# Kernel optimization log

Hardware: AMD Instinct MI355X
Metric: run time of the kernel (lower is better)

## Reference

```python
import jax, jax.numpy as jnp
import numpy as np

N = 20000   # nodes
E = 640000  # edges
F = 128     # input feature dim
H1 = 64     # hidden1
H2 = 32     # hidden2 (forced by Bilinear(32,32,1))
R = 65      # num_relations / num classes
B = 4096    # query pairs


def rgcn_conv(x, src, dst, etype, W, Wroot, b):
    """PyG RGCNConv with aggr='mean': out_i = sum_r mean_{j in N_r(i)} x_j @ W_r + x_i @ Wroot + b."""
    n, f = x.shape
    seg = dst * R + etype                      # combined (node, relation) segment id
    msgs = x[src]                              # [E, f] gather
    agg = jax.ops.segment_sum(msgs, seg, num_segments=n * R).reshape(n, R, f)
    cnt = jax.ops.segment_sum(jnp.ones((msgs.shape[0],), x.dtype), seg, num_segments=n * R).reshape(n, R, 1)
    mean = agg / jnp.maximum(cnt, 1.0)         # mean per relation, zero where no edges
    out = jnp.einsum('nrf,rfo->no', mean, W) + x @ Wroot + b
    return out


def bilinear(h, c, w, b):
    # torch.nn.Bilinear(32,32,1): w [1,32,32], b [1]
    return jnp.einsum('nh,hk,nk->n', h, w[0], c)[:, None] + b


def setup_inputs():
    key = jax.random.key(0)
    ks = jax.random.split(key, 20)
    inp = {}
    inp['x_o'] = jax.random.normal(ks[0], (N, F), jnp.float32)
    inp['x_a'] = jax.random.normal(ks[1], (N, F), jnp.float32)
    inp['edge_index'] = jax.random.randint(ks[2], (2, E), 0, N, dtype=jnp.int32)
    inp['e_type'] = jax.random.randint(ks[3], (E,), 0, R, dtype=jnp.int32)
    inp['e_type1'] = jax.random.randint(ks[4], (E,), 0, R, dtype=jnp.int32)
    inp['idx'] = jax.random.randint(ks[5], (2, B), 0, N, dtype=jnp.int32)
    # RGCN layer 1
    s1 = 1.0 / np.sqrt(F)
    inp['W1'] = jax.random.normal(ks[6], (R, F, H1), jnp.float32) * s1
    inp['root1'] = jax.random.normal(ks[7], (F, H1), jnp.float32) * s1
    inp['b1'] = jnp.zeros((H1,), jnp.float32)
    # RGCN layer 2
    s2 = 1.0 / np.sqrt(H1)
    inp['W2'] = jax.random.normal(ks[8], (R, H1, H2), jnp.float32) * s2
    inp['root2'] = jax.random.normal(ks[9], (H1, H2), jnp.float32) * s2
    inp['b2'] = jnp.zeros((H2,), jnp.float32)
    # attention mix, discriminator, classifier
    inp['attt'] = jnp.array([0.5, 0.5], jnp.float32)
    inp['disc_w'] = jax.random.normal(ks[10], (1, H2, H2), jnp.float32) * (1.0 / np.sqrt(H2))
    inp['disc_b'] = jnp.zeros((1,), jnp.float32)
    cin = 2 * (H1 + H2)
    inp['cls_w'] = jax.random.normal(ks[11], (cin, R), jnp.float32) * (1.0 / np.sqrt(cin))
    inp['cls_b'] = jnp.zeros((R,), jnp.float32)
    return inp


def reference(x_o, x_a, edge_index, e_type, e_type1, idx,
              W1, root1, b1, W2, root2, b2, attt, disc_w, disc_b, cls_w, cls_b):
    src, dst = edge_index[0], edge_index[1]
    # three encoder passes (dropout is identity at eval)
    x1_o = jax.nn.relu(rgcn_conv(x_o, src, dst, e_type, W1, root1, b1))
    x2_o = rgcn_conv(x1_o, src, dst, e_type, W2, root2, b2)

    x1_a = jax.nn.relu(rgcn_conv(x_a, src, dst, e_type, W1, root1, b1))
    x2_o_a = rgcn_conv(x1_a, src, dst, e_type, W2, root2, b2)

    x1_aa = jax.nn.relu(rgcn_conv(x_o, src, dst, e_type1, W1, root1, b1))
    x2_o_a_a = rgcn_conv(x1_aa, src, dst, e_type1, W2, root2, b2)

    # readout + sigmoid, expanded summary vector
    h_os = jax.nn.sigmoid(jnp.mean(x2_o, axis=0))        # [H2]
    c_x = jnp.broadcast_to(h_os, x2_o.shape)             # [N, H2]
    ret_os = jnp.concatenate([bilinear(x2_o, c_x, disc_w, disc_b),
                              bilinear(x2_o_a, c_x, disc_w, disc_b)], axis=1)
    ret_os_a = jnp.concatenate([bilinear(x2_o, c_x, disc_w, disc_b),
                                bilinear(x2_o_a_a, c_x, disc_w, disc_b)], axis=1)

    final = jnp.concatenate([attt[0] * x1_o, attt[1] * x2_o], axis=1)  # [N, H1+H2]
    entity1 = final[idx[0]]
    entity2 = final[idx[1]]
    concat = jnp.concatenate([entity1, entity2], axis=1)  # [B, 2*(H1+H2)]
    log = concat @ cls_w + cls_b                           # [B, 65]
    return (log, ret_os, ret_os_a, x2_o)
```

## Files before the change

### kernel.cpp

```cpp
#include <hip/hip_runtime.h>

#define NN 20000
#define NE 640000
#define FF 128
#define H1 64
#define H2 32
#define RR 65
#define BQ 4096
#define NR (NN*RR)
#define NDPAD 20480

#define SM_HIST_A 0
#define SM_START_A 128
#define SM_CUR_A 256
#define SM_HIST_B 384
#define SM_START_B 512
#define SM_CUR_B 640
#define SM_HACC 768
#define SM_V 832

#define CPB1 32
#define CPB2 32

typedef __attribute__((ext_vector_type(8))) short bhalf8;
typedef __attribute__((ext_vector_type(4))) float f32x4;
#define MFMA16(a, b, c) __builtin_amdgcn_mfma_f32_16x16x32_bf16(a, b, c, 0, 0, 0)

__device__ __forceinline__ unsigned short f2bf(float f) {
  unsigned int u = __float_as_uint(f);
  unsigned int r = (u + 0x7fffu + ((u >> 16) & 1u)) >> 16;
  return (unsigned short)r;
}
__device__ __forceinline__ float bf2f(unsigned short u) {
  return __uint_as_float((unsigned)u << 16);
}
__device__ __forceinline__ void atomPK(unsigned short* p, unsigned v) {
  asm volatile("global_atomic_pk_add_bf16 %0, %1, off"
               :: "v"((unsigned long long)p), "v"(v) : "memory");
}

__global__ __launch_bounds__(256) void k_hist(
    const int* __restrict__ ei, const int* __restrict__ etA, const int* __restrict__ etB,
    int* __restrict__ cntA, int* __restrict__ cntB, int* __restrict__ sm,
    int* __restrict__ cntD) {
  __shared__ int lh[2 * RR];
  int tid = threadIdx.x;
  for (int i = tid; i < 2 * RR; i += blockDim.x) lh[i] = 0;
  __syncthreads();
  int e = blockIdx.x * blockDim.x + tid;
  if (e < NE) {
    int dst = ei[NE + e];
    int ta = etA[e], tb = etB[e];
    atomicAdd(&cntA[dst * RR + ta], 1);
    atomicAdd(&cntB[dst * RR + tb], 1);
    atomicAdd(&cntD[dst], 1);
    atomicAdd(&lh[ta], 1);
    atomicAdd(&lh[RR + tb], 1);
  }
  __syncthreads();
  for (int i = tid; i < 2 * RR; i += blockDim.x) {
    int c = lh[i];
    if (c) atomicAdd(&sm[(i < RR) ? (SM_HIST_A + i) : (SM_HIST_B + (i - RR))], c);
  }
}

__global__ __launch_bounds__(128) void k_prefix(int* __restrict__ sm) {
  int w = threadIdx.x >> 6;
  if ((threadIdx.x & 63) == 0 && w < 2) {
    int hb = w ? SM_HIST_B : SM_HIST_A;
    int sb = w ? SM_START_B : SM_START_A;
    int cb = w ? SM_CUR_B : SM_CUR_A;
    int h[RR];
#pragma unroll
    for (int r = 0; r < RR; ++r) h[r] = sm[hb + r];
    int s = 0;
#pragma unroll
    for (int r = 0; r < RR; ++r) { sm[sb + r] = s; sm[cb + r] = s; s += h[r]; }
  }
}

__global__ __launch_bounds__(256) void k_prefixD(
    const int* __restrict__ cntD, int* __restrict__ startD,
    int* __restrict__ curA, int* __restrict__ curB) {
  __shared__ int psum[256];
  __shared__ int pbase[257];
  int t = threadIdx.x;
  int c0 = t * 80;
  int c1 = (c0 + 80 < NN) ? (c0 + 80) : NN;
  int s = 0;
  for (int i = c0; i < c1; ++i) s += cntD[i];
  psum[t] = s;
  __syncthreads();
  if (t == 0) {
    int a = 0;
    for (int i = 0; i < 256; ++i) { pbase[i] = a; a += psum[i]; }
    pbase[256] = a;
  }
  __syncthreads();
  int run = pbase[t];
  for (int i = c0; i < c1; ++i) {
    startD[i] = run; curA[i] = run; curB[i] = run;
    run += cntD[i];
  }
  if (t == 255) startD[NN] = pbase[256];
}

__global__ __launch_bounds__(256) void k_scatter(
    const int* __restrict__ etA, const int* __restrict__ etB,
    int* __restrict__ sm, int* __restrict__ ordA, int* __restrict__ ordB) {
  __shared__ int lhA[RR], lbA[RR], lhB[RR], lbB[RR];
  int tid = threadIdx.x;
  for (int i = tid; i < RR; i += blockDim.x) { lhA[i] = 0; lhB[i] = 0; }
  __syncthreads();
  int e = blockIdx.x * blockDim.x + tid;
  int ta = 0, tb = 0, ra = 0, rb = 0;
  bool valid = (e < NE);
  if (valid) {
    ta = etA[e]; tb = etB[e];
    ra = atomicAdd(&lhA[ta], 1);
    rb = atomicAdd(&lhB[tb], 1);
  }
  __syncthreads();
  for (int i = tid; i < RR; i += blockDim.x) {
    if (lhA[i]) lbA[i] = atomicAdd(&sm[SM_CUR_A + i], lhA[i]);
    if (lhB[i]) lbB[i] = atomicAdd(&sm[SM_CUR_B + i], lhB[i]);
  }
  __syncthreads();
  if (valid) { ordA[lbA[ta] + ra] = e; ordB[lbB[tb] + rb] = e; }
}

__global__ __launch_bounds__(256) void k_emeta(
    const int* __restrict__ ei, const int* __restrict__ ordA, const int* __restrict__ ordB,
    const int* __restrict__ cntA, const int* __restrict__ cntB,
    const int* __restrict__ etA, const int* __restrict__ etB,
    int2* __restrict__ sdA, float* __restrict__ ivA,
    int2* __restrict__ sdB, float* __restrict__ ivB) {
  int p = blockIdx.x * blockDim.x + threadIdx.x;
  if (p >= NE) return;
  {
    int e = ordA[p]; int s = ei[e], d = ei[NE + e]; int t = etA[e];
    sdA[p] = make_int2(s, d);
    ivA[p] = 1.0f / (float)cntA[(size_t)d * RR + t];
  }
  {
    int e = ordB[p]; int s = ei[e], d = ei[NE + e]; int t = etB[e];
    sdB[p] = make_int2(s, d);
    ivB[p] = 1.0f / (float)cntB[(size_t)d * RR + t];
  }
}

__global__ __launch_bounds__(256) void k_scatterD(
    const int2* __restrict__ sdA, const int2* __restrict__ sdB,
    int* __restrict__ curA, int* __restrict__ curB,
    int* __restrict__ posA, int* __restrict__ posB) {
  int p = blockIdx.x * blockDim.x + threadIdx.x;
  if (p >= NE) return;
  posA[atomicAdd(&curA[sdA[p].y], 1)] = p;
  posB[atomicAdd(&curB[sdB[p].y], 1)] = p;
}

__global__ __launch_bounds__(256) void k_cvt2(const float4* __restrict__ inA,
                                              const float4* __restrict__ inB,
                                              uint4* __restrict__ outA,
                                              uint4* __restrict__ outB, int n8) {
  int i = blockIdx.x * blockDim.x + threadIdx.x;
  if (i >= 2 * n8) return;
  const float4* in = (i < n8) ? inA : inB;
  uint4* out = (i < n8) ? outA : outB;
  int j = (i < n8) ? i : i - n8;
  float4 a = in[2 * j], b = in[2 * j + 1];
  uint4 o;
  o.x = (unsigned)f2bf(a.x) | ((unsigned)f2bf(a.y) << 16);
  o.y = (unsigned)f2bf(a.z) | ((unsigned)f2bf(a.w) << 16);
  o.z = (unsigned)f2bf(b.x) | ((unsigned)f2bf(b.y) << 16);
  o.w = (unsigned)f2bf(b.z) | ((unsigned)f2bf(b.w) << 16);
  out[j] = o;
}

__global__ __launch_bounds__(256) void k_relu16(uint4* __restrict__ a, int n4) {
  int i = blockIdx.x * blockDim.x + threadIdx.x;
  if (i >= n4) return;
  uint4 u = a[i];
  unsigned* w = (unsigned*)&u;
#pragma unroll
  for (int t = 0; t < 4; ++t) {
    unsigned lo = (w[t] & 0x8000u) ? 0u : (w[t] & 0xFFFFu);
    unsigned hi = (w[t] & 0x80000000u) ? 0u : (w[t] & 0xFFFF0000u);
    w[t] = lo | hi;
  }
  a[i] = u;
}

__global__ __launch_bounds__(256) void k_wprep1(const float* __restrict__ W,
                                                unsigned short* __restrict__ Wf) {
  int r = blockIdx.x;
  int lane = threadIdx.x & 63, w = threadIdx.x >> 6;
#pragma unroll
  for (int s4 = 0; s4 < 4; ++s4) {
    int slot = w * 4 + s4;
    int ks = slot >> 2, n = slot & 3;
    int krow = ks * 32 + ((lane >> 4) << 3);
    int colo = n * 16 + (lane & 15);
    unsigned short* o = Wf + (((size_t)r * 16 + slot) * 64 + lane) * 8;
#pragma unroll
    for (int j = 0; j < 8; ++j)
      o[j] = f2bf(W[((size_t)r * FF + krow + j) * H1 + colo]);
  }
}

__global__ __launch_bounds__(256) void k_wprep2(const float* __restrict__ W,
                                                unsigned short* __restrict__ Wf) {
  int r = blockIdx.x;
  int lane = threadIdx.x & 63, slot = threadIdx.x >> 6;
  int ks = slot >> 1, n = slot & 1;
  int krow = ks * 32 + ((lane >> 4) << 3);
  int colo = n * 16 + (lane & 15);
  unsigned short* o = Wf + (((size_t)r * 4 + slot) * 64 + lane) * 8;
#pragma unroll
  for (int j = 0; j < 8; ++j)
    o[j] = f2bf(W[((size_t)r * H1 + krow + j) * H2 + colo]);
}

__global__ __launch_bounds__(256) void k_root1(
    const float* __restrict__ xo, const float* __restrict__ xa,
    const float* __restrict__ rt, const float* __restrict__ b,
    unsigned short* __restrict__ yo, unsigned short* __restrict__ yaa,
    unsigned short* __restrict__ ya) {
  int lane = threadIdx.x & 63;
  int n = (blockIdx.x * blockDim.x + threadIdx.x) >> 6;
  if (n >= NN) return;
  const float4* xo4 = (const float4*)(xo + (size_t)n * FF);
  const float4* xa4 = (const float4*)(xa + (size_t)n * FF);
  float so = b[lane], sa = so;
#pragma unroll
  for (int j = 0; j < FF / 4; ++j) {
    float vo[4], va[4];
    *(float4*)vo = xo4[j];
    *(float4*)va = xa4[j];
#pragma unroll
    for (int t = 0; t < 4; ++t) {
      float wv = rt[(4 * j + t) * H1 + lane];
      so = fmaf(vo[t], wv, so);
      sa = fmaf(va[t], wv, sa);
    }
  }
  yo[(size_t)n * H1 + lane] = f2bf(so);
  yaa[(size_t)n * H1 + lane] = f2bf(so);
  ya[(size_t)n * H1 + lane] = f2bf(sa);
}

#define LM(G, SD, IV)                                       \
  {                                                         \
    const int base_ = s0 + ((G) << 4);                      \
    const int lim_ = cnt - ((G) << 4);                      \
    const int off_ = base_ + ((col < lim_) ? col : 0);      \
    SD = sdp[off_];                                         \
    IV = (col < lim_) ? invp[off_] : 0.f;                   \
  }

#define MFMA_BODY1(A0, A1, A2, A3)                                  \
  f32x4 c0 = {0.f,0.f,0.f,0.f}, c1 = c0, c2 = c0, c3 = c0;          \
  c0 = MFMA16(A0, wb[0], c0);  c1 = MFMA16(A0, wb[1], c1);          \
  c2 = MFMA16(A0, wb[2], c2);  c3 = MFMA16(A0, wb[3], c3);          \
  c0 = MFMA16(A1, wb[4], c0);  c1 = MFMA16(A1, wb[5], c1);          \
  c2 = MFMA16(A1, wb[6], c2);  c3 = MFMA16(A1, wb[7], c3);          \
  c0 = MFMA16(A2, wb[8], c0);  c1 = MFMA16(A2, wb[9], c1);          \
  c2 = MFMA16(A2, wb[10], c2); c3 = MFMA16(A2, wb[11], c3);         \
  c0 = MFMA16(A3, wb[12], c0); c1 = MFMA16(A3, wb[13], c1);         \
  c2 = MFMA16(A3, wb[14], c2); c3 = MFMA16(A3, wb[15], c3);

template <int NIN>
__global__ __launch_bounds__(256, 2) void k_edge1m(
    const int2* __restrict__ sdp, const float* __restrict__ invp,
    const int* __restrict__ sm, int startOff, int histOff,
    const unsigned short* __restrict__ Wf,
    const unsigned short* __restrict__ x16A, const unsigned short* __restrict__ x16B,
    unsigned short* __restrict__ yA, unsigned short* __restrict__ yB) {
  const int r = blockIdx.x / CPB1;
  const int lane = threadIdx.x & 63;
  bhalf8 wb[16];
  {
    const bhalf8* wf = (const bhalf8*)Wf + ((size_t)r * 16) * 64 + lane;
#pragma unroll
    for (int s = 0; s < 16; ++s) wb[s] = wf[(size_t)s * 64];
  }
  const int wvid = (blockIdx.x - r * CPB1) * 4 + (threadIdx.x >> 6);
  const int stride = CPB1 * 4;
  const int s0 = sm[startOff + r];
  const int cnt = sm[histOff + r];
  const int ngroups = (cnt + 15) >> 4;
  if (wvid >= ngroups) return;
  const int cg = lane >> 4;
  const int col = lane & 15;
  const int row0 = cg << 2;

  int2 sdC; float ivC;
  LM(wvid, sdC, ivC);
  for (int G = wvid; G < ngroups; G += stride) {
    int2 sdN = sdC; float ivN = ivC;
    if (G + stride < ngroups) LM(G + stride, sdN, ivN);
    const int src = sdC.x;
    const int dstv = sdC.y;
    const int d0 = __shfl(dstv, row0),     d1 = __shfl(dstv, row0 + 1),
              d2 = __shfl(dstv, row0 + 2), d3 = __shfl(dstv, row0 + 3);
    const float i0 = __shfl(ivC, row0),     i1 = __shfl(ivC, row0 + 1),
                i2 = __shfl(ivC, row0 + 2), i3 = __shfl(ivC, row0 + 3);
#define SCAT1(Y, CCN, NOFF)                                                     \
    {                                                                           \
      float v0 = (CCN)[0] * i0, v1 = (CCN)[1] * i1,                             \
            v2 = (CCN)[2] * i2, v3 = (CCN)[3] * i3;                             \
      float p0 = __shfl_xor(v0, 1), p1 = __shfl_xor(v1, 1),                     \
            p2 = __shfl_xor(v2, 1), p3 = __shfl_xor(v3, 1);                     \
      if (!(lane & 1)) {                                                        \
        atomPK(Y + (size_t)d0 * H1 + (NOFF) + col, (unsigned)f2bf(v0) | ((unsigned)f2bf(p0) << 16)); \
        atomPK(Y + (size_t)d1 * H1 + (NOFF) + col, (unsigned)f2bf(v1) | ((unsigned)f2bf(p1) << 16)); \
        atomPK(Y + (size_t)d2 * H1 + (NOFF) + col, (unsigned)f2bf(v2) | ((unsigned)f2bf(p2) << 16)); \
        atomPK(Y + (size_t)d3 * H1 + (NOFF) + col, (unsigned)f2bf(v3) | ((unsigned)f2bf(p3) << 16)); \
      }                                                                         \
    }
    {
      const bhalf8* xr = (const bhalf8*)x16A + ((size_t)src << 4);
      bhalf8 a0 = xr[cg], a1 = xr[4 + cg], a2 = xr[8 + cg], a3 = xr[12 + cg];
      MFMA_BODY1(a0, a1, a2, a3)
      SCAT1(yA, c0, 0); SCAT1(yA, c1, 16); SCAT1(yA, c2, 32); SCAT1(yA, c3, 48);
    }
    if constexpr (NIN == 2) {
      const bhalf8* xr = (const bhalf8*)x16B + ((size_t)src << 4);
      bhalf8 a0 = xr[cg], a1 = xr[4 + cg], a2 = xr[8 + cg], a3 = xr[12 + cg];
      MFMA_BODY1(a0, a1, a2, a3)
      SCAT1(yB, c0, 0); SCAT1(yB, c1, 16); SCAT1(yB, c2, 32); SCAT1(yB, c3, 48);
    }
#undef SCAT1
    sdC = sdN; ivC = ivN;
  }
}

template <int NIN>
__global__ __launch_bounds__(256, 2) void k_edge1s(
    const int2* __restrict__ sdp, const float* __restrict__ invp,
    const int* __restrict__ sm, int startOff, int histOff,
    const unsigned short* __restrict__ Wf,
    const unsigned short* __restrict__ x16A, const unsigned short* __restrict__ x16B,
    unsigned short* __restrict__ tA, unsigned short* __restrict__ tB) {
  const int r = blockIdx.x / CPB1;
  const int lane = threadIdx.x & 63;
  bhalf8 wb[16];
  {
    const bhalf8* wf = (const bhalf8*)Wf + ((size_t)r * 16) * 64 + lane;
#pragma unroll
    for (int s = 0; s < 16; ++s) wb[s] = wf[(size_t)s * 64];
  }
  const int wvid = (blockIdx.x - r * CPB1) * 4 + (threadIdx.x >> 6);
  const int stride = CPB1 * 4;
  const int s0 = sm[startOff + r];
  const int cnt = sm[histOff + r];
  const int ngroups = (cnt + 15) >> 4;
  if (wvid >= ngroups) return;
  const int cg = lane >> 4;
  const int col = lane & 15;
  const int row0 = cg << 2;

  int2 sdC; float ivC;
  LM(wvid, sdC, ivC);
  for (int G = wvid; G < ngroups; G += stride) {
    int2 sdN = sdC; float ivN = ivC;
    if (G + stride < ngroups) LM(G + stride, sdN, ivN);
    const int src = sdC.x;
    const int base = s0 + (G << 4);
    const int lim = cnt - (G << 4);
    const float i0 = __shfl(ivC, row0),     i1 = __shfl(ivC, row0 + 1),
                i2 = __shfl(ivC, row0 + 2), i3 = __shfl(ivC, row0 + 3);
#define STOR1(T, CCN, NOFF)                                                     \
    {                                                                           \
      float v0 = (CCN)[0] * i0, v1 = (CCN)[1] * i1,                             \
            v2 = (CCN)[2] * i2, v3 = (CCN)[3] * i3;                             \
      float p0 = __shfl_xor(v0, 1), p1 = __shfl_xor(v1, 1),                     \
            p2 = __shfl_xor(v2, 1), p3 = __shfl_xor(v3, 1);                     \
      if (!(lane & 1)) {                                                        \
        if (row0 + 0 < lim) *(unsigned*)(T + (size_t)(base + row0 + 0) * H1 + (NOFF) + col) = (unsigned)f2bf(v0) | ((unsigned)f2bf(p0) << 16); \
        if (row0 + 1 < lim) *(unsigned*)(T + (size_t)(base + row0 + 1) * H1 + (NOFF) + col) = (unsigned)f2bf(v1) | ((unsigned)f2bf(p1) << 16); \
        if (row0 + 2 < lim) *(unsigned*)(T + (size_t)(base + row0 + 2) * H1 + (NOFF) + col) = (unsigned)f2bf(v2) | ((unsigned)f2bf(p2) << 16); \
        if (row0 + 3 < lim) *(unsigned*)(T + (size_t)(base + row0 + 3) * H1 + (NOFF) + col) = (unsigned)f2bf(v3) | ((unsigned)f2bf(p3) << 16); \
      }                                                                         \
    }
    {
      const bhalf8* xr = (const bhalf8*)x16A + ((size_t)src << 4);
      bhalf8 a0 = xr[cg], a1 = xr[4 + cg], a2 = xr[8 + cg], a3 = xr[12 + cg];
      MFMA_BODY1(a0, a1, a2, a3)
      STOR1(tA, c0, 0); STOR1(tA, c1, 16); STOR1(tA, c2, 32); STOR1(tA, c3, 48);
    }
    if constexpr (NIN == 2) {
      const bhalf8* xr = (const bhalf8*)x16B + ((size_t)src << 4);
      bhalf8 a0 = xr[cg], a1 = xr[4 + cg], a2 = xr[8 + cg], a3 = xr[12 + cg];
      MFMA_BODY1(a0, a1, a2, a3)
      STOR1(tB, c0, 0); STOR1(tB, c1, 16); STOR1(tB, c2, 32); STOR1(tB, c3, 48);
    }
#undef STOR1
    sdC = sdN; ivC = ivN;
  }
}

template <int NT>
__global__ __launch_bounds__(256) void k_reduce1(
    const int* __restrict__ startD, const int* __restrict__ pos,
    const unsigned short* __restrict__ t0, const unsigned short* __restrict__ t1,
    const unsigned short* __restrict__ r0, const unsigned short* __restrict__ r1,
    unsigned short* __restrict__ y0, unsigned short* __restrict__ y1) {
  int lane = threadIdx.x & 63;
  int d = (blockIdx.x * blockDim.x + threadIdx.x) >> 6;
  if (d >= NN) return;
  int e0 = startD[d], e1 = startD[d + 1];
  float a0 = 0.f, a1 = 0.f;
  int j = e0;
  for (; j + 4 <= e1; j += 4) {
    int p0 = pos[j], p1 = pos[j + 1], p2 = pos[j + 2], p3 = pos[j + 3];
    a0 += bf2f(t0[(size_t)p0 * H1 + lane]) + bf2f(t0[(size_t)p1 * H1 + lane])
        + bf2f(t0[(size_t)p2 * H1 + lane]) + bf2f(t0[(size_t)p3 * H1 + lane]);
    if constexpr (NT == 2)
      a1 += bf2f(t1[(size_t)p0 * H1 + lane]) + bf2f(t1[(size_t)p1 * H1 + lane])
          + bf2f(t1[(size_t)p2 * H1 + lane]) + bf2f(t1[(size_t)p3 * H1 + lane]);
  }
  for (; j < e1; ++j) {
    int p = pos[j];
    a0 += bf2f(t0[(size_t)p * H1 + lane]);
    if constexpr (NT == 2) a1 += bf2f(t1[(size_t)p * H1 + lane]);
  }
  size_t o = (size_t)d * H1 + lane;
  y0[o] = f2bf(fmaxf(bf2f(r0[o]) + a0, 0.f));
  if constexpr (NT == 2) y1[o] = f2bf(fmaxf(bf2f(r1[o]) + a1, 0.f));
}

__global__ __launch_bounds__(256) void k_root2x3(
    const unsigned short* __restrict__ x1o, const unsigned short* __restrict__ x1a,
    const unsigned short* __restrict__ x1aa,
    const float* __restrict__ rt, const float* __restrict__ b,
    unsigned short* __restrict__ y0, unsigned short* __restrict__ y1,
    unsigned short* __restrict__ y2) {
  int i = blockIdx.x * blockDim.x + threadIdx.x;
  if (i >= NN * H2) return;
  int o = i & (H2 - 1);
  int n = i >> 5;
  const uint2* p0 = (const uint2*)(x1o + (size_t)n * H1);
  const uint2* p1 = (const uint2*)(x1a + (size_t)n * H1);
  const uint2* p2 = (const uint2*)(x1aa + (size_t)n * H1);
  float s0 = b[o], s1 = s0, s2 = s0;
#pragma unroll
  for (int j = 0; j < 16; ++j) {
    uint2 u0 = p0[j], u1 = p1[j], u2 = p2[j];
#pragma unroll
    for (int t = 0; t < 4; ++t) {
      unsigned w0 = (t < 2) ? u0.x : u0.y;
      unsigned w1 = (t < 2) ? u1.x : u1.y;
      unsigned w2 = (t < 2) ? u2.x : u2.y;
      int sh = (t & 1) * 16;
      float wv = rt[(4 * j + t) * H2 + o];
      s0 = fmaf(bf2f((unsigned short)(w0 >> sh)), wv, s0);
      s1 = fmaf(bf2f((unsigned short)(w1 >> sh)), wv, s1);
      s2 = fmaf(bf2f((unsigned short)(w2 >> sh)), wv, s2);
    }
  }
  y0[i] = f2bf(s0); y1[i] = f2bf(s1); y2[i] = f2bf(s2);
}

template <int NIN>
__global__ __launch_bounds__(256, 2) void k_edge2m(
    const int2* __restrict__ sdp, const float* __restrict__ invp,
    const int* __restrict__ sm, int startOff, int histOff,
    const unsigned short* __restrict__ Wf,
    const unsigned short* __restrict__ x16A, const unsigned short* __restrict__ x16B,
    unsigned short* __restrict__ yA, unsigned short* __restrict__ yB) {
  const int r = blockIdx.x / CPB2;
  const int lane = threadIdx.x & 63;
  bhalf8 wb[4];
  {
    const bhalf8* wf = (const bhalf8*)Wf + ((size_t)r * 4) * 64 + lane;
#pragma unroll
    for (int s = 0; s < 4; ++s) wb[s] = wf[(size_t)s * 64];
  }
  const int wvid = (blockIdx.x - r * CPB2) * 4 + (threadIdx.x >> 6);
  const int stride = CPB2 * 4;
  const int s0 = sm[startOff + r];
  const int cnt = sm[histOff + r];
  const int ngroups = (cnt + 15) >> 4;
  if (wvid >= ngroups) return;
  const int cg = lane >> 4;
  const int col = lane & 15;
  const int row0 = cg << 2;

  int2 sdC; float ivC;
  LM(wvid, sdC, ivC);
  for (int G = wvid; G < ngroups; G += stride) {
    int2 sdN = sdC; float ivN = ivC;
    if (G + stride < ngroups) LM(G + stride, sdN, ivN);
    const int src = sdC.x;
    const int dstv = sdC.y;
    const int d0 = __shfl(dstv, row0),     d1 = __shfl(dstv, row0 + 1),
              d2 = __shfl(dstv, row0 + 2), d3 = __shfl(dstv, row0 + 3);
    const float i0 = __shfl(ivC, row0),     i1 = __shfl(ivC, row0 + 1),
                i2 = __shfl(ivC, row0 + 2), i3 = __shfl(ivC, row0 + 3);
#define SCAT2(Y, CCN, NOFF)                                                     \
    {                                                                           \
      float v0 = (CCN)[0] * i0, v1 = (CCN)[1] * i1,                             \
            v2 = (CCN)[2] * i2, v3 = (CCN)[3] * i3;                             \
      float p0 = __shfl_xor(v0, 1), p1 = __shfl_xor(v1, 1),                     \
            p2 = __shfl_xor(v2, 1), p3 = __shfl_xor(v3, 1);                     \
      if (!(lane & 1)) {                                                        \
        atomPK(Y + (size_t)d0 * H2 + (NOFF) + col, (unsigned)f2bf(v0) | ((unsigned)f2bf(p0) << 16)); \
        atomPK(Y + (size_t)d1 * H2 + (NOFF) + col, (unsigned)f2bf(v1) | ((unsigned)f2bf(p1) << 16)); \
        atomPK(Y + (size_t)d2 * H2 + (NOFF) + col, (unsigned)f2bf(v2) | ((unsigned)f2bf(p2) << 16)); \
        atomPK(Y + (size_t)d3 * H2 + (NOFF) + col, (unsigned)f2bf(v3) | ((unsigned)f2bf(p3) << 16)); \
      }                                                                         \
    }
    {
      const bhalf8* xr = (const bhalf8*)x16A + ((size_t)src << 3);
      bhalf8 a0 = xr[cg], a1 = xr[4 + cg];
      f32x4 c0 = {0.f,0.f,0.f,0.f}, c1 = c0;
      c0 = MFMA16(a0, wb[0], c0); c1 = MFMA16(a0, wb[1], c1);
      c0 = MFMA16(a1, wb[2], c0); c1 = MFMA16(a1, wb[3], c1);
      SCAT2(yA, c0, 0); SCAT2(yA, c1, 16);
    }
    if constexpr (NIN == 2) {
      const bhalf8* xr = (const bhalf8*)x16B + ((size_t)src << 3);
      bhalf8 a0 = xr[cg], a1 = xr[4 + cg];
      f32x4 c0 = {0.f,0.f,0.f,0.f}, c1 = c0;
      c0 = MFMA16(a0, wb[0], c0); c1 = MFMA16(a0, wb[1], c1);
      c0 = MFMA16(a1, wb[2], c0); c1 = MFMA16(a1, wb[3], c1);
      SCAT2(yB, c0, 0); SCAT2(yB, c1, 16);
    }
#undef SCAT2
    sdC = sdN; ivC = ivN;
  }
}

template <int NIN>
__global__ __launch_bounds__(256, 2) void k_edge2s(
    const int2* __restrict__ sdp, const float* __restrict__ invp,
    const int* __restrict__ sm, int startOff, int histOff,
    const unsigned short* __restrict__ Wf,
    const unsigned short* __restrict__ x16A, const unsigned short* __restrict__ x16B,
    unsigned short* __restrict__ tA, unsigned short* __restrict__ tB) {
  const int r = blockIdx.x / CPB2;
  const int lane = threadIdx.x & 63;
  bhalf8 wb[4];
  {
    const bhalf8* wf = (const bhalf8*)Wf + ((size_t)r * 4) * 64 + lane;
#pragma unroll
    for (int s = 0; s < 4; ++s) wb[s] = wf[(size_t)s * 64];
  }
  const int wvid = (blockIdx.x - r * CPB2) * 4 + (threadIdx.x >> 6);
  const int stride = CPB2 * 4;
  const int s0 = sm[startOff + r];
  const int cnt = sm[histOff + r];
  const int ngroups = (cnt + 15) >> 4;
  if (wvid >= ngroups) return;
  const int cg = lane >> 4;
  const int col = lane & 15;
  const int row0 = cg << 2;

  int2 sdC; float ivC;
  LM(wvid, sdC, ivC);
  for (int G = wvid; G < ngroups; G += stride) {
    int2 sdN = sdC; float ivN = ivC;
    if (G + stride < ngroups) LM(G + stride, sdN, ivN);
    const int src = sdC.x;
    const int base = s0 + (G << 4);
    const int lim = cnt - (G << 4);
    const float i0 = __shfl(ivC, row0),     i1 = __shfl(ivC, row0 + 1),
                i2 = __shfl(ivC, row0 + 2), i3 = __shfl(ivC, row0 + 3);
#define STOR2(T, CCN, NOFF)                                                     \
    {                                                                           \
      float v0 = (CCN)[0] * i0, v1 = (CCN)[1] * i1,                             \
            v2 = (CCN)[2] * i2, v3 = (CCN)[3] * i3;                             \
      float p0 = __shfl_xor(v0, 1), p1 = __shfl_xor(v1, 1),                     \
            p2 = __shfl_xor(v2, 1), p3 = __shfl_xor(v3, 1);                     \
      if (!(lane & 1)) {                                                        \
        if (row0 + 0 < lim) *(unsigned*)(T + (size_t)(base + row0 + 0) * H2 + (NOFF) + col) = (unsigned)f2bf(v0) | ((unsigned)f2bf(p0) << 16); \
        if (row0 + 1 < lim) *(unsigned*)(T + (size_t)(base + row0 + 1) * H2 + (NOFF) + col) = (unsigned)f2bf(v1) | ((unsigned)f2bf(p1) << 16); \
        if (row0 + 2 < lim) *(unsigned*)(T + (size_t)(base + row0 + 2) * H2 + (NOFF) + col) = (unsigned)f2bf(v2) | ((unsigned)f2bf(p2) << 16); \
        if (row0 + 3 < lim) *(unsigned*)(T + (size_t)(base + row0 + 3) * H2 + (NOFF) + col) = (unsigned)f2bf(v3) | ((unsigned)f2bf(p3) << 16); \
      }                                                                         \
    }
    {
      const bhalf8* xr = (const bhalf8*)x16A + ((size_t)src << 3);
      bhalf8 a0 = xr[cg], a1 = xr[4 + cg];
      f32x4 c0 = {0.f,0.f,0.f,0.f}, c1 = c0;
      c0 = MFMA16(a0, wb[0], c0); c1 = MFMA16(a0, wb[1], c1);
      c0 = MFMA16(a1, wb[2], c0); c1 = MFMA16(a1, wb[3], c1);
      STOR2(tA, c0, 0); STOR2(tA, c1, 16);
    }
    if constexpr (NIN == 2) {
      const bhalf8* xr = (const bhalf8*)x16B + ((size_t)src << 3);
      bhalf8 a0 = xr[cg], a1 = xr[4 + cg];
      f32x4 c0 = {0.f,0.f,0.f,0.f}, c1 = c0;
      c0 = MFMA16(a0, wb[0], c0); c1 = MFMA16(a0, wb[1], c1);
      c0 = MFMA16(a1, wb[2], c0); c1 = MFMA16(a1, wb[3], c1);
      STOR2(tB, c0, 0); STOR2(tB, c1, 16);
    }
#undef STOR2
    sdC = sdN; ivC = ivN;
  }
}

template <int NT>
__global__ __launch_bounds__(256) void k_reduce2(
    const int* __restrict__ startD, const int* __restrict__ pos,
    const unsigned short* __restrict__ t0, const unsigned short* __restrict__ t1,
    const unsigned short* __restrict__ r0, const unsigned short* __restrict__ r1,
    unsigned short* __restrict__ y0, unsigned short* __restrict__ y1,
    float* __restrict__ f32out) {
  int gt = blockIdx.x * blockDim.x + threadIdx.x;
  int d = gt >> 5;
  int colc = gt & 31;
  if (d >= NN) return;
  int e0 = startD[d], e1 = startD[d + 1];
  float a0 = 0.f, a1 = 0.f;
  int j = e0;
  for (; j + 4 <= e1; j += 4) {
    int p0 = pos[j], p1 = pos[j + 1], p2 = pos[j + 2], p3 = pos[j + 3];
    a0 += bf2f(t0[(size_t)p0 * H2 + colc]) + bf2f(t0[(size_t)p1 * H2 + colc])
        + bf2f(t0[(size_t)p2 * H2 + colc]) + bf2f(t0[(size_t)p3 * H2 + colc]);
    if constexpr (NT == 2)
      a1 += bf2f(t1[(size_t)p0 * H2 + colc]) + bf2f(t1[(size_t)p1 * H2 + colc])
          + bf2f(t1[(size_t)p2 * H2 + colc]) + bf2f(t1[(size_t)p3 * H2 + colc]);
  }
  for (; j < e1; ++j) {
    int p = pos[j];
    a0 += bf2f(t0[(size_t)p * H2 + colc]);
    if constexpr (NT == 2) a1 += bf2f(t1[(size_t)p * H2 + colc]);
  }
  size_t o = (size_t)d * H2 + colc;
  float v0 = bf2f(r0[o]) + a0;
  y0[o] = f2bf(v0);
  if (f32out) f32out[o] = v0;
  if constexpr (NT == 2) y1[o] = f2bf(bf2f(r1[o]) + a1);
}

__global__ __launch_bounds__(256) void k_fin(const uint4* __restrict__ xb,
                                             float4* __restrict__ out, int n8) {
  int i = blockIdx.x * blockDim.x + threadIdx.x;
  if (i >= n8) return;
  uint4 u = xb[i];
  float4 a, b;
  a.x = bf2f((unsigned short)u.x); a.y = bf2f((unsigned short)(u.x >> 16));
  a.z = bf2f((unsigned short)u.y); a.w = bf2f((unsigned short)(u.y >> 16));
  b.x = bf2f((unsigned short)u.z); b.y = bf2f((unsigned short)(u.z >> 16));
  b.z = bf2f((unsigned short)u.w); b.w = bf2f((unsigned short)(u.w >> 16));
  out[2 * i] = a; out[2 * i + 1] = b;
}

__global__ __launch_bounds__(256) void k_colsum(const float* __restrict__ x2o,
                                                float* __restrict__ hacc) {
  int tid = threadIdx.x;
  int col = tid & 31;
  int rgrp = blockIdx.x * (blockDim.x >> 5) + (tid >> 5);
  int nth = gridDim.x * (blockDim.x >> 5);
  float s = 0.f;
  for (int n = rgrp; n < NN; n += nth) s += x2o[(size_t)n * H2 + col];
  unsafeAtomicAdd(&hacc[col], s);
}

__global__ __launch_bounds__(64) void k_disc(const float* __restrict__ hacc,
                                             const float* __restrict__ dw,
                                             float* __restrict__ vout) {
  __shared__ float hos[H2];
  int t = threadIdx.x;
  if (t < H2) hos[t] = 1.0f / (1.0f + expf(-hacc[t] / (float)NN));
  __syncthreads();
  if (t < H2) {
    float s = 0.f;
#pragma unroll
    for (int k = 0; k < H2; ++k) s = fmaf(dw[t * H2 + k], hos[k], s);
    vout[t] = s;
  }
}

__global__ __launch_bounds__(256) void k_ret(
    const unsigned short* __restrict__ x2o, const unsigned short* __restrict__ x2oa,
    const unsigned short* __restrict__ x2oaa,
    const float* __restrict__ v, const float* __restrict__ db,
    float* __restrict__ ros, float* __restrict__ rosa) {
  int n = blockIdx.x * blockDim.x + threadIdx.x;
  if (n >= NN) return;
  const uint2* a2 = (const uint2*)(x2o + (size_t)n * H2);
  const uint2* b2 = (const uint2*)(x2oa + (size_t)n * H2);
  const uint2* c2 = (const uint2*)(x2oaa + (size_t)n * H2);
  const float4* v4 = (const float4*)v;
  float r0 = 0.f, r1 = 0.f, r2 = 0.f;
#pragma unroll
  for (int j = 0; j < 8; ++j) {
    uint2 ua = a2[j], ub = b2[j], uc = c2[j];
    float4 vv = v4[j];
    r0 += bf2f((unsigned short)ua.x) * vv.x + bf2f((unsigned short)(ua.x >> 16)) * vv.y
        + bf2f((unsigned short)ua.y) * vv.z + bf2f((unsigned short)(ua.y >> 16)) * vv.w;
    r1 += bf2f((unsigned short)ub.x) * vv.x + bf2f((unsigned short)(ub.x >> 16)) * vv.y
        + bf2f((unsigned short)ub.y) * vv.z + bf2f((unsigned short)(ub.y >> 16)) * vv.w;
    r2 += bf2f((unsigned short)uc.x) * vv.x + bf2f((unsigned short)(uc.x >> 16)) * vv.y
        + bf2f((unsigned short)uc.y) * vv.z + bf2f((unsigned short)(uc.y >> 16)) * vv.w;
  }
  float bb = db[0];
  ros[n * 2] = r0 + bb;  ros[n * 2 + 1] = r1 + bb;
  rosa[n * 2] = r0 + bb; rosa[n * 2 + 1] = r2 + bb;
}

__global__ __launch_bounds__(128) void k_cls(
    const int* __restrict__ idx, const unsigned short* __restrict__ x1o,
    const float* __restrict__ x2o,
    const float* __restrict__ attt, const float* __restrict__ cw, const float* __restrict__ cb,
    float* __restrict__ lg) {
  int b = blockIdx.x;
  int r = threadIdx.x;
  if (r >= RR) return;
  int i1 = idx[b], i2 = idx[BQ + b];
  float a0 = attt[0], a1 = attt[1];
  float acc = cb[r];
  const uint2* q1 = (const uint2*)(x1o + (size_t)i1 * H1);
  const float4* q2 = (const float4*)(x2o + (size_t)i1 * H2);
  const uint2* q3 = (const uint2*)(x1o + (size_t)i2 * H1);
  const float4* q4 = (const float4*)(x2o + (size_t)i2 * H2);
#pragma unroll
  for (int j = 0; j < 16; ++j) {
    uint2 u = q1[j];
    float v0 = bf2f((unsigned short)u.x), v1 = bf2f((unsigned short)(u.x >> 16));
    float v2 = bf2f((unsigned short)u.y), v3 = bf2f((unsigned short)(u.y >> 16));
    acc = fmaf(a0 * v0, cw[(4 * j) * RR + r], acc);
    acc = fmaf(a0 * v1, cw[(4 * j + 1) * RR + r], acc);
    acc = fmaf(a0 * v2, cw[(4 * j + 2) * RR + r], acc);
    acc = fmaf(a0 * v3, cw[(4 * j + 3) * RR + r], acc);
  }
#pragma unroll
  for (int j = 0; j < H2 / 4; ++j) {
    float v[4]; *(float4*)v = q2[j];
#pragma unroll
    for (int t = 0; t < 4; ++t) acc = fmaf(a1 * v[t], cw[(H1 + 4 * j + t) * RR + r], acc);
  }
#pragma unroll
  for (int j = 0; j < 16; ++j) {
    uint2 u = q3[j];
    float v0 = bf2f((unsigned short)u.x), v1 = bf2f((unsigned short)(u.x >> 16));
    float v2 = bf2f((unsigned short)u.y), v3 = bf2f((unsigned short)(u.y >> 16));
    acc = fmaf(a0 * v0, cw[(96 + 4 * j) * RR + r], acc);
    acc = fmaf(a0 * v1, cw[(96 + 4 * j + 1) * RR + r], acc);
    acc = fmaf(a0 * v2, cw[(96 + 4 * j + 2) * RR + r], acc);
    acc = fmaf(a0 * v3, cw[(96 + 4 * j + 3) * RR + r], acc);
  }
#pragma unroll
  for (int j = 0; j < H2 / 4; ++j) {
    float v[4]; *(float4*)v = q4[j];
#pragma unroll
    for (int t = 0; t < 4; ++t) acc = fmaf(a1 * v[t], cw[(96 + H1 + 4 * j + t) * RR + r], acc);
  }
  lg[(size_t)b * RR + r] = acc;
}

extern "C" void kernel_launch(void* const* d_in, const int* in_sizes, int n_in,
                              void* d_out, int out_size, void* d_ws, size_t ws_size,
                              hipStream_t stream) {
  const float* x_o  = (const float*)d_in[0];
  const float* x_a  = (const float*)d_in[1];
  const int*   ei   = (const int*)d_in[2];
  const int*   etA  = (const int*)d_in[3];
  const int*   etB  = (const int*)d_in[4];
  const int*   idx  = (const int*)d_in[5];
  const float* W1   = (const float*)d_in[6];
  const float* rt1  = (const float*)d_in[7];
  const float* b1   = (const float*)d_in[8];
  const float* W2   = (const float*)d_in[9];
  const float* rt2  = (const float*)d_in[10];
  const float* b2   = (const float*)d_in[11];
  const float* attt = (const float*)d_in[12];
  const float* dw   = (const float*)d_in[13];
  const float* db   = (const float*)d_in[14];
  const float* cw   = (const float*)d_in[15];
  const float* cb   = (const float*)d_in[16];

  const size_t NRp = 1300224;
  int* wsI    = (int*)d_ws;
  int* cntA   = wsI;
  int* cntB   = cntA + NRp;
  int* sm     = cntB + NRp;
  int* cntD   = sm + 1024;
  int* startD = cntD + NDPAD;
  int* curA   = startD + NDPAD;
  int* curB   = curA + NDPAD;
  int* ordA   = curB + NDPAD;
  int* ordB   = ordA + NE;
  int* posA   = ordB + NE;
  int* posB   = posA + NE;
  int2*  sdA  = (int2*)(posB + NE);
  float* ivA  = (float*)(sdA + NE);
  int2*  sdB  = (int2*)(ivA + NE);
  float* ivB  = (float*)(sdB + NE);
  unsigned short* x1o16   = (unsigned short*)(ivB + NE);
  unsigned short* x1a16   = x1o16 + (size_t)NN * H1;
  unsigned short* x1aa16  = x1a16 + (size_t)NN * H1;
  unsigned short* x2ob    = x1aa16 + (size_t)NN * H1;
  unsigned short* x2oab   = x2ob + (size_t)NN * H2;
  unsigned short* x2oaab  = x2oab + (size_t)NN * H2;
  unsigned short* xo16    = x2oaab + (size_t)NN * H2;
  unsigned short* xa16    = xo16 + (size_t)NN * FF;
  unsigned short* W1f     = xa16 + (size_t)NN * FF;
  unsigned short* W2f     = W1f + (size_t)RR * 16 * 64 * 8;
  unsigned short* rootO16 = W2f + (size_t)RR * 4 * 64 * 8;
  unsigned short* rootA16 = rootO16 + (size_t)NN * H1;
  unsigned short* r2o16   = rootA16 + (size_t)NN * H1;
  unsigned short* r2a16   = r2o16 + (size_t)NN * H2;
  unsigned short* r2aa16  = r2a16 + (size_t)NN * H2;
  unsigned short* t0      = r2aa16 + (size_t)NN * H2;
  unsigned short* t1      = t0 + (size_t)NE * H1;
  unsigned short* tc1     = t0 + (size_t)NE * H2;

  const size_t ofsT = (size_t)((char*)t0 - (char*)d_ws);
  const size_t needFull = ofsT + (size_t)2 * NE * H1 * 2 + 256;
  const size_t needMid  = ofsT + (size_t)2 * NE * H2 * 2 + 256;
  const bool fullT = ws_size >= needFull;
  const bool midT  = fullT || ws_size >= needMid;

  float* smF  = (float*)sm;
  float* hacc = smF + SM_HACC;
  float* vbuf = smF + SM_V;

  float* outF   = (float*)d_out;
  float* o_log  = outF;
  float* o_ros  = outF + (size_t)BQ * RR;
  float* o_rosa = o_ros + (size_t)NN * 2;
  float* o_x2o  = o_rosa + (size_t)NN * 2;

  hipMemsetAsync(wsI, 0, (2 * NRp + 1024 + NDPAD) * sizeof(int), stream);

  k_cvt2<<<(2 * NN * FF / 8 + 255) / 256, 256, 0, stream>>>(
      (const float4*)x_o, (const float4*)x_a, (uint4*)xo16, (uint4*)xa16, NN * FF / 8);
  k_wprep1<<<RR, 256, 0, stream>>>(W1, W1f);
  k_wprep2<<<RR, 256, 0, stream>>>(W2, W2f);

  k_hist<<<(NE + 255) / 256, 256, 0, stream>>>(ei, etA, etB, cntA, cntB, sm, cntD);
  k_prefix<<<1, 128, 0, stream>>>(sm);
  k_scatter<<<(NE + 255) / 256, 256, 0, stream>>>(etA, etB, sm, ordA, ordB);
  k_emeta<<<(NE + 255) / 256, 256, 0, stream>>>(ei, ordA, ordB, cntA, cntB,
                                                etA, etB, sdA, ivA, sdB, ivB);
  if (midT) {
    k_prefixD<<<1, 256, 0, stream>>>(cntD, startD, curA, curB);
    k_scatterD<<<(NE + 255) / 256, 256, 0, stream>>>(sdA, sdB, curA, curB, posA, posB);
  }

  if (fullT) {
    k_root1<<<(NN * H1) / 256, 256, 0, stream>>>(x_o, x_a, rt1, b1,
                                                 rootO16, rootO16, rootA16);
    k_edge1s<2><<<RR * CPB1, 256, 0, stream>>>(sdA, ivA, sm, SM_START_A, SM_HIST_A,
                                               W1f, xo16, xa16, t0, t1);
    k_reduce1<2><<<(NN * 64) / 256, 256, 0, stream>>>(startD, posA, t0, t1,
                                                      rootO16, rootA16, x1o16, x1a16);
    k_edge1s<1><<<RR * CPB1, 256, 0, stream>>>(sdB, ivB, sm, SM_START_B, SM_HIST_B,
                                               W1f, xo16, nullptr, t0, nullptr);
    k_reduce1<1><<<(NN * 64) / 256, 256, 0, stream>>>(startD, posB, t0, nullptr,
                                                      rootO16, nullptr, x1aa16, nullptr);
  } else {
    k_root1<<<(NN * H1) / 256, 256, 0, stream>>>(x_o, x_a, rt1, b1,
                                                 x1o16, x1aa16, x1a16);
    k_edge1m<2><<<RR * CPB1, 256, 0, stream>>>(sdA, ivA, sm, SM_START_A, SM_HIST_A,
                                               W1f, xo16, xa16, x1o16, x1a16);
    k_edge1m<1><<<RR * CPB1, 256, 0, stream>>>(sdB, ivB, sm, SM_START_B, SM_HIST_B,
                                               W1f, xo16, nullptr, x1aa16, nullptr);
    k_relu16<<<(3 * NN * H1 / 8 + 255) / 256, 256, 0, stream>>>((uint4*)x1o16,
                                                                3 * NN * H1 / 8);
  }

  if (midT) {
    k_root2x3<<<(NN * H2 + 255) / 256, 256, 0, stream>>>(x1o16, x1a16, x1aa16, rt2, b2,
                                                         r2o16, r2a16, r2aa16);
    k_edge2s<2><<<RR * CPB2, 256, 0, stream>>>(sdA, ivA, sm, SM_START_A, SM_HIST_A,
                                               W2f, x1o16, x1a16, t0, tc1);
    k_reduce2<2><<<(NN * 32) / 256, 256, 0, stream>>>(startD, posA, t0, tc1,
                                                      r2o16, r2a16, x2ob, x2oab, o_x2o);
    k_edge2s<1><<<RR * CPB2, 256, 0, stream>>>(sdB, ivB, sm, SM_START_B, SM_HIST_B,
                                               W2f, x1aa16, nullptr, t0, nullptr);
    k_reduce2<1><<<(NN * 32) / 256, 256, 0, stream>>>(startD, posB, t0, nullptr,
                                                      r2aa16, nullptr, x2oaab, nullptr,
                                                      nullptr);
  } else {
    k_root2x3<<<(NN * H2 + 255) / 256, 256, 0, stream>>>(x1o16, x1a16, x1aa16, rt2, b2,
                                                         x2ob, x2oab, x2oaab);
    k_edge2m<2><<<RR * CPB2, 256, 0, stream>>>(sdA, ivA, sm, SM_START_A, SM_HIST_A,
                                               W2f, x1o16, x1a16, x2ob, x2oab);
    k_edge2m<1><<<RR * CPB2, 256, 0, stream>>>(sdB, ivB, sm, SM_START_B, SM_HIST_B,
                                               W2f, x1aa16, nullptr, x2oaab, nullptr);
    k_fin<<<(NN * H2 / 8 + 255) / 256, 256, 0, stream>>>((const uint4*)x2ob,
                                                         (float4*)o_x2o, NN * H2 / 8);
  }

  k_colsum<<<128, 256, 0, stream>>>(o_x2o, hacc);
  k_disc<<<1, 64, 0, stream>>>(hacc, dw, vbuf);
  k_ret<<<(NN + 255) / 256, 256, 0, stream>>>(x2ob, x2oab, x2oaab, vbuf, db, o_ros, o_rosa);
  k_cls<<<BQ, 128, 0, stream>>>(idx, x1o16, o_x2o, attt, cw, cb, o_log);
}
```

Baseline: 866.9 us.

## Replace dense per-(node,relation) count arrays with per-destination inverse-count computation

Removes the two dense N*R count arrays, along with their large memset and the scattered atomics into them. The relation type is now packed into the high bits of the source index, and the per-edge inverse mean count is computed in a new kernel. That kernel walks each destination's edge list, one wavefront per node, and counts edges of matching relation with shuffles. The cost is extra kernel launches and work that grows with the square of each node's degree, and the destination CSR build now always runs.

Result: faster. 828.1 us (-4.5%).

```diff
diff --git a/kernel.cpp b/kernel.cpp
--- a/kernel.cpp
+++ b/kernel.cpp
@@ -7,7 +7,6 @@
 #define H2 32
 #define RR 65
 #define BQ 4096
-#define NR (NN*RR)
 #define NDPAD 20480
 
 #define SM_HIST_A 0
@@ -41,8 +40,7 @@
 
 __global__ __launch_bounds__(256) void k_hist(
     const int* __restrict__ ei, const int* __restrict__ etA, const int* __restrict__ etB,
-    int* __restrict__ cntA, int* __restrict__ cntB, int* __restrict__ sm,
-    int* __restrict__ cntD) {
+    int* __restrict__ sm, int* __restrict__ cntD) {
   __shared__ int lh[2 * RR];
   int tid = threadIdx.x;
   for (int i = tid; i < 2 * RR; i += blockDim.x) lh[i] = 0;
@@ -50,12 +48,9 @@
   int e = blockIdx.x * blockDim.x + tid;
   if (e < NE) {
     int dst = ei[NE + e];
-    int ta = etA[e], tb = etB[e];
-    atomicAdd(&cntA[dst * RR + ta], 1);
-    atomicAdd(&cntB[dst * RR + tb], 1);
     atomicAdd(&cntD[dst], 1);
-    atomicAdd(&lh[ta], 1);
-    atomicAdd(&lh[RR + tb], 1);
+    atomicAdd(&lh[etA[e]], 1);
+    atomicAdd(&lh[RR + etB[e]], 1);
   }
   __syncthreads();
   for (int i = tid; i < 2 * RR; i += blockDim.x) {
@@ -131,21 +126,17 @@
 
 __global__ __launch_bounds__(256) void k_emeta(
     const int* __restrict__ ei, const int* __restrict__ ordA, const int* __restrict__ ordB,
-    const int* __restrict__ cntA, const int* __restrict__ cntB,
     const int* __restrict__ etA, const int* __restrict__ etB,
-    int2* __restrict__ sdA, float* __restrict__ ivA,
-    int2* __restrict__ sdB, float* __restrict__ ivB) {
+    int2* __restrict__ sdA, int2* __restrict__ sdB) {
   int p = blockIdx.x * blockDim.x + threadIdx.x;
   if (p >= NE) return;
   {
-    int e = ordA[p]; int s = ei[e], d = ei[NE + e]; int t = etA[e];
-    sdA[p] = make_int2(s, d);
-    ivA[p] = 1.0f / (float)cntA[(size_t)d * RR + t];
+    int e = ordA[p];
+    sdA[p] = make_int2(ei[e] | (etA[e] << 20), ei[NE + e]);
   }
   {
-    int e = ordB[p]; int s = ei[e], d = ei[NE + e]; int t = etB[e];
-    sdB[p] = make_int2(s, d);
-    ivB[p] = 1.0f / (float)cntB[(size_t)d * RR + t];
+    int e = ordB[p];
+    sdB[p] = make_int2(ei[e] | (etB[e] << 20), ei[NE + e]);
   }
 }
 
@@ -157,6 +148,30 @@
   if (p >= NE) return;
   posA[atomicAdd(&curA[sdA[p].y], 1)] = p;
   posB[atomicAdd(&curB[sdB[p].y], 1)] = p;
+}
+
+__global__ __launch_bounds__(256) void k_invD(
+    const int* __restrict__ startD, const int* __restrict__ pos,
+    const int2* __restrict__ sd, float* __restrict__ iv) {
+  int lane = threadIdx.x & 63;
+  int d = (blockIdx.x * blockDim.x + threadIdx.x) >> 6;
+  if (d >= NN) return;
+  int e0 = startD[d], e1 = startD[d + 1];
+  int len = e1 - e0;
+  for (int c0 = 0; c0 < len; c0 += 64) {
+    int myj = c0 + lane;
+    int myp = 0, myrel = -1;
+    if (myj < len) { myp = pos[e0 + myj]; myrel = ((unsigned)sd[myp].x) >> 20; }
+    int cnt = 0;
+    for (int c1 = 0; c1 < len; c1 += 64) {
+      int oj = c1 + lane;
+      int orel = (oj < len) ? (int)(((unsigned)sd[pos[e0 + oj]].x) >> 20) : -2;
+      int kmax = (len - c1 < 64) ? (len - c1) : 64;
+      for (int k = 0; k < kmax; ++k)
+        cnt += (__shfl(orel, k) == myrel);
+    }
+    if (myj < len) iv[myp] = 1.0f / (float)cnt;
+  }
 }
 
 __global__ __launch_bounds__(256) void k_cvt2(const float4* __restrict__ inA,
@@ -299,7 +314,7 @@
   for (int G = wvid; G < ngroups; G += stride) {
     int2 sdN = sdC; float ivN = ivC;
     if (G + stride < ngroups) LM(G + stride, sdN, ivN);
-    const int src = sdC.x;
+    const int src = sdC.x & 0xFFFFF;
     const int dstv = sdC.y;
     const int d0 = __shfl(dstv, row0),     d1 = __shfl(dstv, row0 + 1),
               d2 = __shfl(dstv, row0 + 2), d3 = __shfl(dstv, row0 + 3);
@@ -365,7 +380,7 @@
   for (int G = wvid; G < ngroups; G += stride) {
     int2 sdN = sdC; float ivN = ivC;
     if (G + stride < ngroups) LM(G + stride, sdN, ivN);
-    const int src = sdC.x;
+    const int src = sdC.x & 0xFFFFF;
     const int base = s0 + (G << 4);
     const int lim = cnt - (G << 4);
     const float i0 = __shfl(ivC, row0),     i1 = __shfl(ivC, row0 + 1),
@@ -492,7 +507,7 @@
   for (int G = wvid; G < ngroups; G += stride) {
     int2 sdN = sdC; float ivN = ivC;
     if (G + stride < ngroups) LM(G + stride, sdN, ivN);
-    const int src = sdC.x;
+    const int src = sdC.x & 0xFFFFF;
     const int dstv = sdC.y;
     const int d0 = __shfl(dstv, row0),     d1 = __shfl(dstv, row0 + 1),
               d2 = __shfl(dstv, row0 + 2), d3 = __shfl(dstv, row0 + 3);
@@ -562,7 +577,7 @@
   for (int G = wvid; G < ngroups; G += stride) {
     int2 sdN = sdC; float ivN = ivC;
     if (G + stride < ngroups) LM(G + stride, sdN, ivN);
-    const int src = sdC.x;
+    const int src = sdC.x & 0xFFFFF;
     const int base = s0 + (G << 4);
     const int lim = cnt - (G << 4);
     const float i0 = __shfl(ivC, row0),     i1 = __shfl(ivC, row0 + 1),
@@ -773,11 +788,8 @@
   const float* cw   = (const float*)d_in[15];
   const float* cb   = (const float*)d_in[16];
 
-  const size_t NRp = 1300224;
   int* wsI    = (int*)d_ws;
-  int* cntA   = wsI;
-  int* cntB   = cntA + NRp;
-  int* sm     = cntB + NRp;
+  int* sm     = wsI;
   int* cntD   = sm + 1024;
   int* startD = cntD + NDPAD;
   int* curA   = startD + NDPAD;
@@ -787,9 +799,9 @@
   int* posA   = ordB + NE;
   int* posB   = posA + NE;
   int2*  sdA  = (int2*)(posB + NE);
-  float* ivA  = (float*)(sdA + NE);
-  int2*  sdB  = (int2*)(ivA + NE);
-  float* ivB  = (float*)(sdB + NE);
+  int2*  sdB  = sdA + NE;
+  float* ivA  = (float*)(sdB + NE);
+  float* ivB  = ivA + NE;
   unsigned short* x1o16   = (unsigned short*)(ivB + NE);
   unsigned short* x1a16   = x1o16 + (size_t)NN * H1;
   unsigned short* x1aa16  = x1a16 + (size_t)NN * H1;
@@ -825,22 +837,21 @@
   float* o_rosa = o_ros + (size_t)NN * 2;
   float* o_x2o  = o_rosa + (size_t)NN * 2;
 
-  hipMemsetAsync(wsI, 0, (2 * NRp + 1024 + NDPAD) * sizeof(int), stream);
+  hipMemsetAsync(wsI, 0, (1024 + NDPAD) * sizeof(int), stream);
 
   k_cvt2<<<(2 * NN * FF / 8 + 255) / 256, 256, 0, stream>>>(
       (const float4*)x_o, (const float4*)x_a, (uint4*)xo16, (uint4*)xa16, NN * FF / 8);
   k_wprep1<<<RR, 256, 0, stream>>>(W1, W1f);
   k_wprep2<<<RR, 256, 0, stream>>>(W2, W2f);
 
-  k_hist<<<(NE + 255) / 256, 256, 0, stream>>>(ei, etA, etB, cntA, cntB, sm, cntD);
+  k_hist<<<(NE + 255) / 256, 256, 0, stream>>>(ei, etA, etB, sm, cntD);
   k_prefix<<<1, 128, 0, stream>>>(sm);
+  k_prefixD<<<1, 256, 0, stream>>>(cntD, startD, curA, curB);
   k_scatter<<<(NE + 255) / 256, 256, 0, stream>>>(etA, etB, sm, ordA, ordB);
-  k_emeta<<<(NE + 255) / 256, 256, 0, stream>>>(ei, ordA, ordB, cntA, cntB,
-                                                etA, etB, sdA, ivA, sdB, ivB);
-  if (midT) {
-    k_prefixD<<<1, 256, 0, stream>>>(cntD, startD, curA, curB);
-    k_scatterD<<<(NE + 255) / 256, 256, 0, stream>>>(sdA, sdB, curA, curB, posA, posB);
-  }
+  k_emeta<<<(NE + 255) / 256, 256, 0, stream>>>(ei, ordA, ordB, etA, etB, sdA, sdB);
+  k_scatterD<<<(NE + 255) / 256, 256, 0, stream>>>(sdA, sdB, curA, curB, posA, posB);
+  k_invD<<<(NN * 64 + 255) / 256, 256, 0, stream>>>(startD, posA, sdA, ivA);
+  k_invD<<<(NN * 64 + 255) / 256, 256, 0, stream>>>(startD, posB, sdB, ivB);
 
   if (fullT) {
     k_root1<<<(NN * H1) / 256, 256, 0, stream>>>(x_o, x_a, rt1, b1,
```
